# Optimization experiments

Measured on AMD Instinct MI355X. Metric: run time of the kernel, lower is better.

## Reference

```python
import jax, jax.numpy as jnp
import numpy as np
import math

B, NK, NQ = 8, 2048, 2048
DK = DQ = DV = 256
H = 1024


def setup_inputs() -> dict:
    key = jax.random.key(0)
    ks = jax.random.split(key, 11)
    def lin(kw, kb, fan_in, fan_out):
        bound = 1.0 / math.sqrt(fan_in)
        W = jax.random.uniform(kw, (fan_out, fan_in), minval=-bound, maxval=bound, dtype=jnp.float32)
        b = jax.random.uniform(kb, (fan_out,), minval=-bound, maxval=bound, dtype=jnp.float32)
        return W, b
    Wk_w, Wk_b = lin(ks[0], ks[1], DK, H)
    Wq_w, Wq_b = lin(ks[2], ks[3], DQ, H)
    Wv_w, Wv_b = lin(ks[4], ks[5], DV, H)
    lin_w, lin_b = lin(ks[6], ks[7], H, DV)
    KEY = jax.random.normal(ks[8], (B, NK, DK), dtype=jnp.float32)
    VALUE = jax.random.normal(ks[9], (B, NK, DV), dtype=jnp.float32)
    QUERY = jax.random.normal(ks[10], (B, NQ, DQ), dtype=jnp.float32)
    return {"KEY": KEY, "VALUE": VALUE, "QUERY": QUERY,
            "Wk_w": Wk_w, "Wk_b": Wk_b, "Wq_w": Wq_w, "Wq_b": Wq_b,
            "Wv_w": Wv_w, "Wv_b": Wv_b, "lin_w": lin_w, "lin_b": lin_b}


def reference(KEY, VALUE, QUERY, Wk_w, Wk_b, Wq_w, Wq_b, Wv_w, Wv_b, lin_w, lin_b):
    # Projections (dropout in eval mode == identity)
    Wk = KEY @ Wk_w.T + Wk_b      # [b, nk, h]
    Wq = QUERY @ Wq_w.T + Wq_b    # [b, nq, h]
    Wv = VALUE @ Wv_w.T + Wv_b    # [b, nk, h]
    scale = 1.0 / math.sqrt(Wq.shape[-1])
    # dist[b, i(key), k(query)]
    dist = jnp.einsum('bih,bkh->bik', Wk, Wq) * scale
    # softmax over the QUERY axis (dim=2), non-standard
    weights = jax.nn.softmax(dist, axis=2)
    # context[b, k(query), h]
    context = jnp.einsum('bik,bih->bkh', weights, Wv)
    res = context @ lin_w.T + lin_b  # [b, nq, input_v]
    return res
```

## Files before the change

### kernel.cpp

```cpp
#include <hip/hip_runtime.h>
#include <hip/hip_bf16.h>

using bf16 = __hip_bfloat16;
typedef __attribute__((ext_vector_type(8))) short s16x8;
typedef __attribute__((ext_vector_type(4))) float f32x4;

__device__ __forceinline__ void async_cp16(const void* g, void* lds) {
    __builtin_amdgcn_global_load_lds(
        (const __attribute__((address_space(1))) unsigned int*)g,
        (__attribute__((address_space(3))) unsigned int*)lds,
        16, 0, 0);
}

__device__ __forceinline__ void storeC(float* p, float v) { *p = v; }
__device__ __forceinline__ void storeC(bf16* p, float v) { *p = __float2bfloat16(v); }

__device__ __forceinline__ s16x8 pack8(float4 a, float4 b) {
    union { bf16 h[8]; s16x8 v; } o;
    o.h[0] = __float2bfloat16(a.x); o.h[1] = __float2bfloat16(a.y);
    o.h[2] = __float2bfloat16(a.z); o.h[3] = __float2bfloat16(a.w);
    o.h[4] = __float2bfloat16(b.x); o.h[5] = __float2bfloat16(b.y);
    o.h[6] = __float2bfloat16(b.z); o.h[7] = __float2bfloat16(b.w);
    return o.v;
}

__global__ __launch_bounds__(256) void prep_kernel(
    const float* __restrict__ Wk_w, const float* __restrict__ Wk_b,
    const float* __restrict__ Wq_w,
    const float* __restrict__ Wv_w, const float* __restrict__ Wv_b,
    const float* __restrict__ lin_w,
    bf16* __restrict__ WkT, bf16* __restrict__ WqT, bf16* __restrict__ WvT,
    bf16* __restrict__ linb, float* __restrict__ csm, float* __restrict__ Cbig)
{
    const int t = threadIdx.x, b = blockIdx.x, y = blockIdx.y;
    if (y <= 2) {
        const float* src = (y == 0) ? Wk_w : (y == 1) ? Wq_w : Wv_w;
        const float* bia = (y == 0) ? Wk_b : Wv_b;
        bf16* dst = (y == 0) ? WkT : (y == 1) ? WqT : WvT;
        if (b < 64) {
            __shared__ float T[64][65];
            const int h0 = (b & 15) * 64, d0 = (b >> 4) * 64;
            const int r = t >> 2, cg = t & 3;
            const float* sp = src + (h0 + r) * 256 + d0 + cg * 16;
#pragma unroll
            for (int c4 = 0; c4 < 4; ++c4) {
                float4 v = *(const float4*)(sp + c4 * 4);
                const int cb = cg * 16 + c4 * 4;
                T[cb + 0][r] = v.x; T[cb + 1][r] = v.y;
                T[cb + 2][r] = v.z; T[cb + 3][r] = v.w;
            }
            __syncthreads();
            union { bf16 h[16]; uint4 u[2]; } o;
#pragma unroll
            for (int j = 0; j < 16; ++j) o.h[j] = __float2bfloat16(T[r][cg * 16 + j]);
            uint4* dp = (uint4*)(dst + (size_t)(d0 + r) * 1024 + h0 + cg * 16);
            dp[0] = o.u[0]; dp[1] = o.u[1];
        } else if (y != 1) {
            if (b < 68) {
                const int i = (b - 64) * 256 + t;
                dst[256 * 1024 + i] = __float2bfloat16(bia[i]);
            } else if (b < 132) {
                const int i = (b - 68) * 256 + t;
                if (i < 127 * 1024 / 8)
                    ((uint4*)(dst + 257 * 1024))[i] = uint4{0, 0, 0, 0};
            }
        }
    } else if (y == 3) {
        const int i = b * 256 + t;
        if (i < 65536) {
            float4 v = ((const float4*)lin_w)[i];
            union { bf16 h[4]; uint2 u; } o;
            o.h[0] = __float2bfloat16(v.x); o.h[1] = __float2bfloat16(v.y);
            o.h[2] = __float2bfloat16(v.z); o.h[3] = __float2bfloat16(v.w);
            ((uint2*)linb)[i] = o.u;
        }
    } else {
        const int i = b * 256 + t;
        if (i < 4096) ((float4*)csm)[i] = float4{0.f, 0.f, 0.f, 0.f};
        if (i < 98304) ((float4*)Cbig)[i] = float4{0.f, 0.f, 0.f, 0.f};
    }
}

template <typename OutT, int BIAS, int BN, int SWZ = 0, int EXP = 0, int CVT = 0,
          int CSDIV = 0, int TM = 4, int BK = 64, int ATOM = 0>
__global__ __launch_bounds__(256) void gemm_nt(
    const void* __restrict__ Av, const void* __restrict__ Bv,
    OutT* __restrict__ C, const float* __restrict__ bias, int bstride,
    float* __restrict__ colsum,
    int M, int N, int K, int ldA, int ldB,
    long long sA, long long sB, long long sC,
    float scale, int nz, int npn)
{
    constexpr int NF = BN / 32;
    constexpr int BM = TM * 32;
    constexpr bool AF = (CVT & 1) != 0, BF = (CVT & 2) != 0;
    constexpr int NC8 = BK / 8;
    constexpr int NC4 = BK / 4;
    constexpr int RPC8 = 256 / NC8;
    constexpr int RPC4 = 256 / NC4;
    static_assert(!EXP || (AF && BN == 128 && TM == 4 && BK == 64), "EXP layout");
    __shared__ __align__(16) char AsRaw[AF ? BM * BK * 4 : BM * BK * 2];
    __shared__ __align__(16) char BsRaw[BF ? BN * BK * 4 : BN * BK * 2];
    bf16*  As  = (bf16*)AsRaw;   float* Asf = (float*)AsRaw;
    bf16*  Bs  = (bf16*)BsRaw;   float* Bsf = (float*)BsRaw;

    int bz, m0, n0;
    if constexpr (SWZ) {
        const int bid = blockIdx.x;
        bz = bid % nz;
        const int t0 = bid / nz;
        const int grp = t0 / (4 * npn);
        m0 = (grp * 4 + (t0 % 4)) * BM;
        n0 = ((t0 / 4) % npn) * BN;
    } else {
        bz = blockIdx.z;
        m0 = blockIdx.y * BM;
        n0 = blockIdx.x * BN;
    }
    C += sC * bz;

    const bf16*  A16 = nullptr; const float* A32 = nullptr;
    const bf16*  B16 = nullptr; const float* B32 = nullptr;
    if constexpr (AF) A32 = (const float*)Av + sA * bz;
    else              A16 = (const bf16*)Av + sA * bz;
    if constexpr (BF) B32 = (const float*)Bv + sB * bz;
    else              B16 = (const bf16*)Bv + sB * bz;

    const int t = threadIdx.x;
    const int lane = t & 63;
    const int w = t >> 6;
    const int wm = (w >> 1) * (BM / 2);
    const int wn = (w & 1) * (BN / 2);

    f32x4 acc[TM][NF] = {};

    const int trow = t / NC8;
    const int tcol = (t % NC8) ^ (trow % NC8);
    const int t4r = t / NC4;
    const int t4c = (t % NC4) ^ (t4r % NC4);
    char* stA = (char*)AsRaw + (size_t)w * 1024;
    char* stB = (char*)BsRaw + (size_t)w * 1024;

    for (int k0 = 0; k0 < K; k0 += BK) {
        __syncthreads();
        if constexpr (AF) {
            const float* a_src = A32 + (long long)(m0 + t4r) * ldA + k0 + t4c * 4;
#pragma unroll
            for (int c = 0; c < BM / RPC4; ++c)
                async_cp16(a_src + (long long)(c * RPC4) * ldA, stA + c * 4096);
        } else {
            const bf16* a_src = A16 + (long long)(m0 + trow) * ldA + k0 + tcol * 8;
#pragma unroll
            for (int c = 0; c < BM / RPC8; ++c)
                async_cp16(a_src + (long long)(c * RPC8) * ldA, stA + c * 4096);
        }
        if constexpr (BF) {
            const float* b_src = B32 + (long long)(n0 + t4r) * ldB + k0 + t4c * 4;
#pragma unroll
            for (int c = 0; c < BN / RPC4; ++c)
                async_cp16(b_src + (long long)(c * RPC4) * ldB, stB + c * 4096);
        } else {
            const bf16* b_src = B16 + (long long)(n0 + trow) * ldB + k0 + tcol * 8;
#pragma unroll
            for (int c = 0; c < BN / RPC8; ++c)
                async_cp16(b_src + (long long)(c * RPC8) * ldB, stB + c * 4096);
        }
        __syncthreads();

        const int rl = lane & 15;
        const int quad = lane >> 4;
#pragma unroll
        for (int kk = 0; kk < BK; kk += 32) {
            const int c8 = (kk >> 3) + quad;
            const int ko = ((c8 ^ (rl & (NC8 - 1))) << 3);
            const int l0 = (kk >> 2) + quad * 2;
            const int k4 = rl & (NC4 - 1);
            s16x8 af[TM], bfr[NF];
#pragma unroll
            for (int i = 0; i < TM; ++i) {
                if constexpr (AF) {
                    const float* rp = Asf + (size_t)(wm + i * 16 + rl) * BK;
                    float4 f0 = *(const float4*)(rp + ((l0 ^ k4) << 2));
                    float4 f1 = *(const float4*)(rp + (((l0 + 1) ^ k4) << 2));
                    af[i] = pack8(f0, f1);
                } else {
                    af[i] = *(const s16x8*)(As + (size_t)(wm + i * 16 + rl) * BK + ko);
                }
            }
#pragma unroll
            for (int j = 0; j < NF; ++j) {
                if constexpr (BF) {
                    const float* rp = Bsf + (size_t)(wn + j * 16 + rl) * BK;
                    float4 f0 = *(const float4*)(rp + ((l0 ^ k4) << 2));
                    float4 f1 = *(const float4*)(rp + (((l0 + 1) ^ k4) << 2));
                    bfr[j] = pack8(f0, f1);
                } else {
                    bfr[j] = *(const s16x8*)(Bs + (size_t)(wn + j * 16 + rl) * BK + ko);
                }
            }
#pragma unroll
            for (int i = 0; i < TM; ++i)
#pragma unroll
                for (int j = 0; j < NF; ++j)
                    acc[i][j] = __builtin_amdgcn_mfma_f32_16x16x32_bf16(
                        af[i], bfr[j], acc[i][j], 0, 0, 0);
        }
    }

    const int cl = lane & 15;
    const int rquad = (lane >> 4) << 2;
    if constexpr (EXP) {
#pragma unroll
        for (int tn = 0; tn < NF; ++tn) {
            const int col = n0 + wn + tn * 16 + cl;
            float csum = 0.f;
#pragma unroll
            for (int tm = 0; tm < TM; ++tm) {
#pragma unroll
                for (int r = 0; r < 4; ++r) {
                    float v = __expf(acc[tm][tn][r] * scale);
                    acc[tm][tn][r] = v;
                    csum += v;
                }
            }
            csum += __shfl_xor(csum, 16);
            csum += __shfl_xor(csum, 32);
            if ((lane >> 4) == 0)
                atomicAdd(&colsum[(long long)bz * N + col], csum);
        }
        float* Ls = (float*)AsRaw;
        const int srow = t >> 3;
        const int scol = (t & 7) * 16;
        const int grb = m0 + ((srow & 16) ? (BM / 2) : 0) + (srow & 15);
#pragma unroll
        for (int tm = 0; tm < TM; ++tm) {
            __syncthreads();
#pragma unroll
            for (int tn = 0; tn < NF; ++tn)
#pragma unroll
                for (int r = 0; r < 4; ++r)
                    Ls[((w >> 1) * 16 + rquad + r) * 132 + wn + tn * 16 + cl] =
                        acc[tm][tn][r];
            __syncthreads();
            float4 f0 = *(const float4*)&Ls[srow * 132 + scol];
            float4 f1 = *(const float4*)&Ls[srow * 132 + scol + 4];
            float4 f2 = *(const float4*)&Ls[srow * 132 + scol + 8];
            float4 f3 = *(const float4*)&Ls[srow * 132 + scol + 12];
            union { s16x8 v; uint4 u; } p0, p1;
            p0.v = pack8(f0, f1);  p1.v = pack8(f2, f3);
            uint4* dst = (uint4*)((bf16*)C + (long long)(grb + tm * 16) * N + n0 + scol);
            dst[0] = p0.u;
            dst[1] = p1.u;
        }
    } else {
#pragma unroll
        for (int tn = 0; tn < NF; ++tn) {
            const int col = n0 + wn + tn * 16 + cl;
            float bcol = 0.f;
            if constexpr (BIAS == 1) bcol = bias[(long long)col * bstride];
            float inv = 1.0f;
            if constexpr (CSDIV == 1) inv = 1.0f / colsum[(long long)bz * N + col];
#pragma unroll
            for (int tm = 0; tm < TM; ++tm) {
#pragma unroll
                for (int r = 0; r < 4; ++r) {
                    const int row = m0 + wm + tm * 16 + rquad + r;
                    float v = acc[tm][tn][r] * scale;
                    if constexpr (BIAS == 1) v += bcol;
                    if constexpr (BIAS == 2) v += bias[(long long)row * bstride];
                    if constexpr (CSDIV == 1) v *= inv;
                    if constexpr (ATOM)
                        atomicAdd((float*)C + (long long)row * N + col, v);
                    else
                        storeC(C + (long long)row * N + col, v);
                }
            }
        }
    }
}

extern "C" void kernel_launch(void* const* d_in, const int* in_sizes, int n_in,
                              void* d_out, int out_size, void* d_ws, size_t ws_size,
                              hipStream_t stream)
{
    constexpr int Bb = 8, NK = 2048, NQ = 2048, D = 256, H = 1024;
    const float scale = 0.03125f;
    constexpr size_t ES  = (size_t)NK * NQ;
    constexpr size_t ET  = (size_t)Bb * NK * D;
    constexpr size_t FIX = 2 * ET * 2
                         + (size_t)512 * 768 * 4
                         + (size_t)512 * 1024 * 2
                         + (size_t)768 * 1024 * 2
                         + (size_t)8 * NK * 4 + 1024;

    const float* KEY   = (const float*)d_in[0];
    const float* VALUE = (const float*)d_in[1];
    const float* QUERY = (const float*)d_in[2];
    const float* Wk_w  = (const float*)d_in[3];
    const float* Wk_b  = (const float*)d_in[4];
    const float* Wq_w  = (const float*)d_in[5];
    const float* Wq_b  = (const float*)d_in[6];
    const float* Wv_w  = (const float*)d_in[7];
    const float* Wv_b  = (const float*)d_in[8];
    const float* lin_w = (const float*)d_in[9];
    const float* lin_b = (const float*)d_in[10];
    float* out = (float*)d_out;
    (void)Wq_b; (void)in_sizes; (void)n_in; (void)out_size;

    auto need = [&](int g) -> size_t { return FIX + (size_t)g * ES * 2; };
    const int g = (ws_size >= need(8)) ? 8 : (ws_size >= need(4)) ? 4 : 2;

    char* ws = (char*)d_ws;
    bf16* Sg   = (bf16*)ws;  ws += (size_t)g * ES * 2;
    bf16* Tp   = (bf16*)ws;  ws += ET * 2;
    bf16* UnT  = (bf16*)ws;  ws += ET * 2;
    float* Cbig= (float*)ws; ws += (size_t)512 * 768 * 4;
    bf16* Abig = (bf16*)ws;  ws += (size_t)512 * 1024 * 2;
    bf16* Bbig = (bf16*)ws;  ws += (size_t)768 * 1024 * 2;
    float* csm = (float*)ws; ws += (size_t)8 * NK * 4;
    bf16* WqT  = Abig;
    bf16* linb = Abig + (size_t)256 * 1024;
    bf16* WkT  = Bbig;
    bf16* WvT  = Bbig + (size_t)384 * 1024;
    const float* C1  = Cbig;
    const float* M2  = Cbig + (size_t)256 * 768 + 384;
    const float* vq  = Cbig + 256;
    const float* c2  = Cbig + (size_t)256 * 768 + 640;

    dim3 blk(256);

    prep_kernel<<<dim3(384, 5), blk, 0, stream>>>(
        Wk_w, Wk_b, Wq_w, Wv_w, Wv_b, lin_w, WkT, WqT, WvT, linb, csm, Cbig);

    gemm_nt<float, 0, 128, 0, 0, 0, 0, 4, 64, 1><<<dim3(6, 4, 4), blk, 0, stream>>>(
        Abig, Bbig, Cbig, nullptr, 1, nullptr, 512, 768, 256, 1024, 1024,
        256, 256, 0, 1.0f, 1, 1);

    gemm_nt<bf16, 1, 64, 1, 0, 3, 0, 2><<<dim3(1024), blk, 0, stream>>>(
        KEY, C1, Tp, vq, 768, nullptr, Bb * NK, D, D, D, 768,
        0, 0, 0, 1.0f, 1, 4);

    for (int b0 = 0; b0 < Bb; b0 += g) {
        gemm_nt<bf16, 0, 128, 1, 1, 1, 1, 4><<<dim3(g * (NQ / 128) * (NK / 128)), blk, 0, stream>>>(
            QUERY + (size_t)b0 * NQ * D, Tp + (size_t)b0 * NK * D, Sg,
            nullptr, 1, csm + (size_t)b0 * NK,
            NQ, NK, D, D, D,
            (long long)NQ * D, (long long)NK * D, (long long)NQ * NK, scale,
            g, NK / 128);
        gemm_nt<bf16, 2, 64, 1, 0, 3, 1, 2><<<dim3((g * NK / 64) * 4), blk, 0, stream>>>(
            M2, VALUE + (size_t)b0 * NK * D, UnT,
            c2, 768, csm + (size_t)b0 * NK,
            256, g * NK, D, 768, D,
            0, 0, 0, 1.0f, 1, g * NK / 64);
        gemm_nt<float, 1, 64, 1, 0, 0, 0, 2, 128><<<dim3(g * (NQ / 64) * (D / 64)), blk, 0, stream>>>(
            Sg, UnT, out + (size_t)b0 * NQ * D,
            lin_b, 1, nullptr,
            NQ, D, NK, NK, g * NK,
            (long long)NQ * NK, (long long)NK, (long long)NQ * D, 1.0f,
            g, D / 64);
    }
}
```

Before: 213.1 us.

## Pre-convert QUERY to bf16 in projection kernel and merge LDS buffers

```diff
diff --git a/kernel.cpp b/kernel.cpp
--- a/kernel.cpp
+++ b/kernel.cpp
@@ -89,7 +89,8 @@
     float* __restrict__ colsum,
     int M, int N, int K, int ldA, int ldB,
     long long sA, long long sB, long long sC,
-    float scale, int nz, int npn)
+    float scale, int nz, int npn,
+    int nblk, const float* __restrict__ xsrc, bf16* __restrict__ xdst)
 {
     constexpr int NF = BN / 32;
     constexpr int BM = TM * 32;
@@ -98,15 +99,31 @@
     constexpr int NC4 = BK / 4;
     constexpr int RPC8 = 256 / NC8;
     constexpr int RPC4 = 256 / NC4;
-    static_assert(!EXP || (AF && BN == 128 && TM == 4 && BK == 64), "EXP layout");
-    __shared__ __align__(16) char AsRaw[AF ? BM * BK * 4 : BM * BK * 2];
-    __shared__ __align__(16) char BsRaw[BF ? BN * BK * 4 : BN * BK * 2];
+    constexpr size_t ABYTES = AF ? (size_t)BM * BK * 4 : (size_t)BM * BK * 2;
+    constexpr size_t BBYTES = BF ? (size_t)BN * BK * 4 : (size_t)BN * BK * 2;
+    constexpr size_t EPIB   = EXP ? (size_t)32 * 132 * 4 : 0;
+    constexpr size_t LDSZ   = (ABYTES + BBYTES) > EPIB ? (ABYTES + BBYTES) : EPIB;
+    static_assert(!EXP || (BN == 128 && TM == 4 && BK == 64), "EXP layout");
+    __shared__ __align__(16) char LdsRaw[LDSZ];
+    char* AsRaw = LdsRaw;
+    char* BsRaw = LdsRaw + ABYTES;
     bf16*  As  = (bf16*)AsRaw;   float* Asf = (float*)AsRaw;
     bf16*  Bs  = (bf16*)BsRaw;   float* Bsf = (float*)BsRaw;
+
+    const int t = threadIdx.x;
 
     int bz, m0, n0;
     if constexpr (SWZ) {
         const int bid = blockIdx.x;
+        if (xdst != nullptr && bid >= nblk) {
+            const int i = (bid - nblk) * 256 + t;
+            float4 v = ((const float4*)xsrc)[i];
+            union { bf16 h[4]; uint2 u; } o;
+            o.h[0] = __float2bfloat16(v.x); o.h[1] = __float2bfloat16(v.y);
+            o.h[2] = __float2bfloat16(v.z); o.h[3] = __float2bfloat16(v.w);
+            ((uint2*)xdst)[i] = o.u;
+            return;
+        }
         bz = bid % nz;
         const int t0 = bid / nz;
         const int grp = t0 / (4 * npn);
@@ -126,7 +143,6 @@
     if constexpr (BF) B32 = (const float*)Bv + sB * bz;
     else              B16 = (const bf16*)Bv + sB * bz;
 
-    const int t = threadIdx.x;
     const int lane = t & 63;
     const int w = t >> 6;
     const int wm = (w >> 1) * (BM / 2);
@@ -138,8 +154,8 @@
     const int tcol = (t % NC8) ^ (trow % NC8);
     const int t4r = t / NC4;
     const int t4c = (t % NC4) ^ (t4r % NC4);
-    char* stA = (char*)AsRaw + (size_t)w * 1024;
-    char* stB = (char*)BsRaw + (size_t)w * 1024;
+    char* stA = AsRaw + (size_t)w * 1024;
+    char* stB = BsRaw + (size_t)w * 1024;
 
     for (int k0 = 0; k0 < K; k0 += BK) {
         __syncthreads();
@@ -228,7 +244,7 @@
             if ((lane >> 4) == 0)
                 atomicAdd(&colsum[(long long)bz * N + col], csum);
         }
-        float* Ls = (float*)AsRaw;
+        float* Ls = (float*)LdsRaw;
         const int srow = t >> 3;
         const int scol = (t & 7) * 16;
         const int grb = m0 + ((srow & 16) ? (BM / 2) : 0) + (srow & 15);
@@ -287,7 +303,7 @@
     const float scale = 0.03125f;
     constexpr size_t ES  = (size_t)NK * NQ;
     constexpr size_t ET  = (size_t)Bb * NK * D;
-    constexpr size_t FIX = 2 * ET * 2
+    constexpr size_t FIX = 3 * ET * 2
                          + (size_t)512 * 768 * 4
                          + (size_t)512 * 1024 * 2
                          + (size_t)768 * 1024 * 2
@@ -314,6 +330,7 @@
     bf16* Sg   = (bf16*)ws;  ws += (size_t)g * ES * 2;
     bf16* Tp   = (bf16*)ws;  ws += ET * 2;
     bf16* UnT  = (bf16*)ws;  ws += ET * 2;
+    bf16* Qb   = (bf16*)ws;  ws += ET * 2;
     float* Cbig= (float*)ws; ws += (size_t)512 * 768 * 4;
     bf16* Abig = (bf16*)ws;  ws += (size_t)512 * 1024 * 2;
     bf16* Bbig = (bf16*)ws;  ws += (size_t)768 * 1024 * 2;
@@ -334,29 +351,29 @@
 
     gemm_nt<float, 0, 128, 0, 0, 0, 0, 4, 64, 1><<<dim3(6, 4, 4), blk, 0, stream>>>(
         Abig, Bbig, Cbig, nullptr, 1, nullptr, 512, 768, 256, 1024, 1024,
-        256, 256, 0, 1.0f, 1, 1);
-
-    gemm_nt<bf16, 1, 64, 1, 0, 3, 0, 2><<<dim3(1024), blk, 0, stream>>>(
+        256, 256, 0, 1.0f, 1, 1, 0, nullptr, nullptr);
+
+    gemm_nt<bf16, 1, 64, 1, 0, 3, 0, 2><<<dim3(1024 + 4096), blk, 0, stream>>>(
         KEY, C1, Tp, vq, 768, nullptr, Bb * NK, D, D, D, 768,
-        0, 0, 0, 1.0f, 1, 4);
+        0, 0, 0, 1.0f, 1, 4, 1024, QUERY, Qb);
 
     for (int b0 = 0; b0 < Bb; b0 += g) {
-        gemm_nt<bf16, 0, 128, 1, 1, 1, 1, 4><<<dim3(g * (NQ / 128) * (NK / 128)), blk, 0, stream>>>(
-            QUERY + (size_t)b0 * NQ * D, Tp + (size_t)b0 * NK * D, Sg,
+        gemm_nt<bf16, 0, 128, 1, 1, 0, 0, 4><<<dim3(g * (NQ / 128) * (NK / 128)), blk, 0, stream>>>(
+            Qb + (size_t)b0 * NQ * D, Tp + (size_t)b0 * NK * D, Sg,
             nullptr, 1, csm + (size_t)b0 * NK,
             NQ, NK, D, D, D,
             (long long)NQ * D, (long long)NK * D, (long long)NQ * NK, scale,
-            g, NK / 128);
+            g, NK / 128, g * (NQ / 128) * (NK / 128), nullptr, nullptr);
         gemm_nt<bf16, 2, 64, 1, 0, 3, 1, 2><<<dim3((g * NK / 64) * 4), blk, 0, stream>>>(
             M2, VALUE + (size_t)b0 * NK * D, UnT,
             c2, 768, csm + (size_t)b0 * NK,
             256, g * NK, D, 768, D,
-            0, 0, 0, 1.0f, 1, g * NK / 64);
+            0, 0, 0, 1.0f, 1, g * NK / 64, (g * NK / 64) * 4, nullptr, nullptr);
         gemm_nt<float, 1, 64, 1, 0, 0, 0, 2, 128><<<dim3(g * (NQ / 64) * (D / 64)), blk, 0, stream>>>(
             Sg, UnT, out + (size_t)b0 * NQ * D,
             lin_b, 1, nullptr,
             NQ, D, NK, NK, g * NK,
             (long long)NQ * NK, (long long)NK, (long long)NQ * D, 1.0f,
-            g, D / 64);
-    }
-}
+            g, D / 64, g * (NQ / 64) * (D / 64), nullptr, nullptr);
+    }
+}
```

New measurement: 204.5 us. 1.04x faster.
